# Kernel tuning notes

Hardware: AMD Instinct MI355X
Metric: run time of the kernel (lower is better)

Reference implementation:

```python
import jax, jax.numpy as jnp
import numpy as np


def setup_inputs() -> dict:
    key = jax.random.key(0)
    k1, k2, k3 = jax.random.split(key, 3)
    B, N, C_IN, C_OUT = 8, 2048, 128, 64
    x = jax.random.normal(k1, (B, N, C_IN), dtype=jnp.float32)
    # Linear(c_in, c_out): weight [c_out, c_in], bias [c_out]
    W_adj = jax.random.normal(k2, (C_OUT, C_IN), dtype=jnp.float32) * (1.0 / np.sqrt(C_IN))
    b_adj = jax.random.normal(k3, (C_OUT,), dtype=jnp.float32) * 0.01
    return {"x": x, "W_adj": W_adj, "b_adj": b_adj}


def reference(x, W_adj, b_adj):
    # e_x = adj_projection(x): [B, N, C_out]
    e_x = jnp.einsum("bnc,oc->bno", x, W_adj) + b_adj
    # The original loop/concat builds all (i, j) pairs and takes per-pair
    # inner products; this is exactly the Gram matrix e_x @ e_x^T.
    lp = jax.nn.relu(jnp.tanh(jnp.einsum("bic,bjc->bij", e_x, e_x)))  # [B, N, N]
    num_neighbours = x.shape[1]
    node_feats = jnp.einsum("bij,bjc->bic", lp, e_x) / num_neighbours
    return node_feats, lp
```

## Files before the change

### kernel.cpp

```cpp
#include <hip/hip_runtime.h>
#include <hip/hip_bf16.h>


#define B_    8
#define N_    2048
#define D_    64
#define CIN_  128

typedef __bf16 bf16x8 __attribute__((ext_vector_type(8)));
typedef float f32x4  __attribute__((ext_vector_type(4)));
typedef float f32x16 __attribute__((ext_vector_type(16)));

union FragU { uint4 u; bf16x8 f; };

static __device__ __forceinline__ bf16x8 ld_frag(const __hip_bfloat16* p) {
    FragU fu; fu.u = *reinterpret_cast<const uint4*>(p); return fu.f;
}

static __device__ __forceinline__ void split8(const float* p, bf16x8& hi, bf16x8& lo) {
    const float4 a = *reinterpret_cast<const float4*>(p);
    const float4 b = *reinterpret_cast<const float4*>(p + 4);
    const float v[8] = {a.x, a.y, a.z, a.w, b.x, b.y, b.z, b.w};
#pragma unroll
    for (int i = 0; i < 8; i++) {
        const __bf16 h = (__bf16)v[i];
        hi[i] = h;
        lo[i] = (__bf16)(v[i] - (float)h);
    }
}

__global__ __launch_bounds__(256) void ex_kernel(
    const float* __restrict__ x,
    const float* __restrict__ W,
    const float* __restrict__ bias,
    __hip_bfloat16* __restrict__ e_hi,
    __hip_bfloat16* __restrict__ e_lo,
    __hip_bfloat16* __restrict__ e_hiT)
{
    __shared__ __align__(16) __hip_bfloat16 sEh[64 * 72];
    __shared__ __align__(16) __hip_bfloat16 sEl[64 * 72];
    __shared__ __align__(16) __hip_bfloat16 sEt[64 * 72];

    const int tid  = threadIdx.x;
    const int w    = tid >> 6;
    const int lane = tid & 63;
    const int quad = lane >> 4;
    const int l16  = lane & 15;
    const int gr0  = blockIdx.x * 64;
    const int m0   = gr0 + w * 16;

    const float* xrow = x + (size_t)(m0 + l16) * CIN_;
    bf16x8 ah[4], al[4];
#pragma unroll
    for (int ks = 0; ks < 4; ks++)
        split8(xrow + ks * 32 + quad * 8, ah[ks], al[ks]);

    f32x4 acc[4];
#pragma unroll
    for (int nt = 0; nt < 4; nt++) acc[nt] = f32x4{0.f, 0.f, 0.f, 0.f};

#pragma unroll
    for (int ks = 0; ks < 4; ks++) {
#pragma unroll
        for (int nt = 0; nt < 4; nt++) {
            bf16x8 wh, wl;
            split8(W + (size_t)(nt * 16 + l16) * CIN_ + ks * 32 + quad * 8, wh, wl);
            acc[nt] = __builtin_amdgcn_mfma_f32_16x16x32_bf16(ah[ks], wh, acc[nt], 0, 0, 0);
            acc[nt] = __builtin_amdgcn_mfma_f32_16x16x32_bf16(ah[ks], wl, acc[nt], 0, 0, 0);
            acc[nt] = __builtin_amdgcn_mfma_f32_16x16x32_bf16(al[ks], wh, acc[nt], 0, 0, 0);
        }
    }

#pragma unroll
    for (int nt = 0; nt < 4; nt++) {
        const int chan = nt * 16 + l16;
        const float bv = bias[chan];
#pragma unroll
        for (int i = 0; i < 4; i++) {
            const int rl = w * 16 + quad * 4 + i;
            const float e = acc[nt][i] + bv;
            const __hip_bfloat16 hi = __float2bfloat16(e);
            const __hip_bfloat16 lo = __float2bfloat16(e - __bfloat162float(hi));
            sEh[rl * 72 + chan] = hi;
            sEl[rl * 72 + chan] = lo;
            sEt[chan * 72 + rl] = hi;
        }
    }
    __syncthreads();

    const int bt = gr0 >> 11, ir0 = gr0 & (N_ - 1);
#pragma unroll
    for (int p = 0; p < 2; p++) {
        const int q = tid + p * 256;
        const int r = q >> 3, c = (q & 7) * 8;
        *(uint4*)(e_hi + (size_t)(gr0 + r) * D_ + c)  = *(const uint4*)(sEh + r * 72 + c);
        *(uint4*)(e_lo + (size_t)(gr0 + r) * D_ + c)  = *(const uint4*)(sEl + r * 72 + c);
        *(uint4*)(e_hiT + ((size_t)bt * D_ + r) * N_ + ir0 + c) = *(const uint4*)(sEt + r * 72 + c);
    }
}

#define LT 136

__global__ __launch_bounds__(512) void fused_kernel(
    const __hip_bfloat16* __restrict__ e_hi,
    const __hip_bfloat16* __restrict__ e_lo,
    const __hip_bfloat16* __restrict__ e_hiT,
    float* __restrict__ out)
{
    __shared__ __align__(16) __hip_bfloat16 sLp[64 * LT];
    __shared__ __align__(16) float sO[8 * 32 * 64];

    const int b   = blockIdx.x;
    const int i0  = blockIdx.y * 64;
    const int tid = threadIdx.x;
    const int w = tid >> 6, lane = tid & 63;
    const int l32 = lane & 31, half = lane >> 5;
    const int quad = lane >> 4, l16 = lane & 15;
    const int g2 = w >> 2, h2 = w & 3;

    const __hip_bfloat16* eih = e_hi + (size_t)(b * N_ + i0 + g2 * 32 + l32) * D_;
    const __hip_bfloat16* eil = e_lo + (size_t)(b * N_ + i0 + g2 * 32 + l32) * D_;
    bf16x8 ahi[4], alo[4];
#pragma unroll
    for (int ks = 0; ks < 4; ks++) {
        ahi[ks] = ld_frag(eih + ks * 16 + half * 8);
        alo[ks] = ld_frag(eil + ks * 16 + half * 8);
    }

    f32x4 o[2][4];
#pragma unroll
    for (int mt = 0; mt < 2; mt++)
#pragma unroll
        for (int nt = 0; nt < 4; nt++) o[mt][nt] = f32x4{0.f, 0.f, 0.f, 0.f};

    float* lp_out = out + (size_t)B_ * N_ * D_;

    const __hip_bfloat16* ejh_base = e_hi + (size_t)(b * N_ + h2 * 32 + l32) * D_;
    const __hip_bfloat16* ejl_base = e_lo + (size_t)(b * N_ + h2 * 32 + l32) * D_;

    bf16x8 bh[4], bl[4];
#pragma unroll
    for (int ks = 0; ks < 4; ks++) {
        bh[ks] = ld_frag(ejh_base + ks * 16 + half * 8);
        bl[ks] = ld_frag(ejl_base + ks * 16 + half * 8);
    }

    for (int jt = 0; jt < 16; jt++) {
        const int j0 = jt * 128;

        f32x16 s = {};
#pragma unroll
        for (int ks = 0; ks < 4; ks++) {
            s = __builtin_amdgcn_mfma_f32_32x32x16_bf16(ahi[ks], bh[ks], s, 0, 0, 0);
            s = __builtin_amdgcn_mfma_f32_32x32x16_bf16(ahi[ks], bl[ks], s, 0, 0, 0);
            s = __builtin_amdgcn_mfma_f32_32x32x16_bf16(alo[ks], bh[ks], s, 0, 0, 0);
        }

        const int jn = ((jt + 1) & 15) * 128;
#pragma unroll
        for (int ks = 0; ks < 4; ks++) {
            bh[ks] = ld_frag(ejh_base + (size_t)jn * D_ + ks * 16 + half * 8);
            bl[ks] = ld_frag(ejl_base + (size_t)jn * D_ + ks * 16 + half * 8);
        }

        bf16x8 bfr[4];
#pragma unroll
        for (int nt = 0; nt < 4; nt++)
            bfr[nt] = ld_frag(e_hiT + ((size_t)b * D_ + nt * 16 + l16) * N_
                              + j0 + h2 * 32 + quad * 8);

#pragma unroll
        for (int r = 0; r < 16; r++) {
            const int rl = (r & 3) + 8 * (r >> 2) + 4 * half;
            const float tc = fmaxf(s[r], 0.0f);
            const float z = __builtin_amdgcn_exp2f(tc * -2.8853900817779268f);
            const float v = (1.0f - z) * __builtin_amdgcn_rcpf(1.0f + z);
            __builtin_nontemporal_store(
                v, lp_out + (size_t)(b * N_ + i0 + g2 * 32 + rl) * N_ + j0 + h2 * 32 + l32);
            sLp[(g2 * 32 + rl) * LT + h2 * 32 + l32] = __float2bfloat16(v);
        }

        __builtin_amdgcn_s_waitcnt(0xc07f);

#pragma unroll
        for (int mt = 0; mt < 2; mt++) {
            const bf16x8 a = ld_frag(sLp + (g2 * 32 + mt * 16 + l16) * LT + h2 * 32 + quad * 8);
#pragma unroll
            for (int nt = 0; nt < 4; nt++)
                o[mt][nt] = __builtin_amdgcn_mfma_f32_16x16x32_bf16(a, bfr[nt], o[mt][nt], 0, 0, 0);
        }
    }

    __syncthreads();
#pragma unroll
    for (int mt = 0; mt < 2; mt++)
#pragma unroll
        for (int nt = 0; nt < 4; nt++)
#pragma unroll
            for (int i = 0; i < 4; i++)
                sO[w * 2048 + (mt * 16 + quad * 4 + i) * 64 + nt * 16 + l16] = o[mt][nt][i];
    __syncthreads();
#pragma unroll
    for (int p = 0; p < 8; p++) {
        const int q = tid + p * 512;
        const int row = q >> 6, chan = q & 63;
        const int gg = row >> 5, rl = row & 31;
        float v = 0.f;
#pragma unroll
        for (int hh = 0; hh < 4; hh++)
            v += sO[(gg * 4 + hh) * 2048 + rl * 64 + chan];
        out[(size_t)(b * N_ + i0 + row) * D_ + chan] = v * (1.0f / 2048.0f);
    }
}

extern "C" void kernel_launch(void* const* d_in, const int* in_sizes, int n_in,
                              void* d_out, int out_size, void* d_ws, size_t ws_size,
                              hipStream_t stream) {
    const float* x    = (const float*)d_in[0];
    const float* W    = (const float*)d_in[1];
    const float* bias = (const float*)d_in[2];
    float* out = (float*)d_out;

    __hip_bfloat16* e_hi  = (__hip_bfloat16*)d_ws;
    __hip_bfloat16* e_lo  = e_hi + (size_t)B_ * N_ * D_;
    __hip_bfloat16* e_hiT = e_lo + (size_t)B_ * N_ * D_;

    ex_kernel<<<dim3(256), dim3(256), 0, stream>>>(x, W, bias, e_hi, e_lo, e_hiT);
    fused_kernel<<<dim3(8, 32), dim3(512), 0, stream>>>(e_hi, e_lo, e_hiT, out);
}
```

Before: 188.7 us.

## Stage lp tile in fp32 shared memory and write it with coalesced vector stores

The fused kernel now handles 32 rows per block and 512 columns per iteration, with each wave owning 64 columns. The lp values are kept in a double-buffered fp32 shared tile and written to global memory as coalesced 16-byte nontemporal row stores, replacing scattered scalar stores. The grid doubles to 512 blocks and the bf16 conversion moves into the A-fragment load. The cost is much more shared memory per block (about 132 KB), which likely limits occupancy to one block per CU, plus an added __syncthreads per iteration.

```diff
diff --git a/kernel.cpp b/kernel.cpp
--- a/kernel.cpp
+++ b/kernel.cpp
@@ -7,6 +7,12 @@
 #define D_    64
 #define CIN_  128
 
+#define BI    32
+#define BJ    512
+#define NJT   (N_ / BJ)
+#define LW    516
+#define SLPB  (BI * LW)
+
 typedef __bf16 bf16x8 __attribute__((ext_vector_type(8)));
 typedef float f32x4  __attribute__((ext_vector_type(4)));
 typedef float f32x16 __attribute__((ext_vector_type(16)));
@@ -27,6 +33,15 @@
         hi[i] = h;
         lo[i] = (__bf16)(v[i] - (float)h);
     }
+}
+
+static __device__ __forceinline__ bf16x8 cvt8(const float* p) {
+    const float4 a = *reinterpret_cast<const float4*>(p);
+    const float4 b = *reinterpret_cast<const float4*>(p + 4);
+    bf16x8 r;
+    r[0] = (__bf16)a.x; r[1] = (__bf16)a.y; r[2] = (__bf16)a.z; r[3] = (__bf16)a.w;
+    r[4] = (__bf16)b.x; r[5] = (__bf16)b.y; r[6] = (__bf16)b.z; r[7] = (__bf16)b.w;
+    return r;
 }
 
 __global__ __launch_bounds__(256) void ex_kernel(
@@ -99,27 +114,24 @@
     }
 }
 
-#define LT 136
-
 __global__ __launch_bounds__(512) void fused_kernel(
     const __hip_bfloat16* __restrict__ e_hi,
     const __hip_bfloat16* __restrict__ e_lo,
     const __hip_bfloat16* __restrict__ e_hiT,
     float* __restrict__ out)
 {
-    __shared__ __align__(16) __hip_bfloat16 sLp[64 * LT];
-    __shared__ __align__(16) float sO[8 * 32 * 64];
+    __shared__ __align__(16) float smem[2 * SLPB];
 
     const int b   = blockIdx.x;
-    const int i0  = blockIdx.y * 64;
+    const int i0  = blockIdx.y * BI;
     const int tid = threadIdx.x;
     const int w = tid >> 6, lane = tid & 63;
     const int l32 = lane & 31, half = lane >> 5;
     const int quad = lane >> 4, l16 = lane & 15;
-    const int g2 = w >> 2, h2 = w & 3;
-
-    const __hip_bfloat16* eih = e_hi + (size_t)(b * N_ + i0 + g2 * 32 + l32) * D_;
-    const __hip_bfloat16* eil = e_lo + (size_t)(b * N_ + i0 + g2 * 32 + l32) * D_;
+    const int cb = w * 64;
+
+    const __hip_bfloat16* eih = e_hi + (size_t)(b * N_ + i0 + l32) * D_;
+    const __hip_bfloat16* eil = e_lo + (size_t)(b * N_ + i0 + l32) * D_;
     bf16x8 ahi[4], alo[4];
 #pragma unroll
     for (int ks = 0; ks < 4; ks++) {
@@ -135,80 +147,107 @@
 
     float* lp_out = out + (size_t)B_ * N_ * D_;
 
-    const __hip_bfloat16* ejh_base = e_hi + (size_t)(b * N_ + h2 * 32 + l32) * D_;
-    const __hip_bfloat16* ejl_base = e_lo + (size_t)(b * N_ + h2 * 32 + l32) * D_;
-
-    bf16x8 bh[4], bl[4];
-#pragma unroll
-    for (int ks = 0; ks < 4; ks++) {
-        bh[ks] = ld_frag(ejh_base + ks * 16 + half * 8);
-        bl[ks] = ld_frag(ejl_base + ks * 16 + half * 8);
-    }
-
-    for (int jt = 0; jt < 16; jt++) {
-        const int j0 = jt * 128;
-
-        f32x16 s = {};
+    const __hip_bfloat16* ejh_base = e_hi + (size_t)(b * N_ + cb + l32) * D_;
+    const __hip_bfloat16* ejl_base = e_lo + (size_t)(b * N_ + cb + l32) * D_;
+
+    bf16x8 bh[2][4], bl[2][4];
+#pragma unroll
+    for (int st = 0; st < 2; st++)
 #pragma unroll
         for (int ks = 0; ks < 4; ks++) {
-            s = __builtin_amdgcn_mfma_f32_32x32x16_bf16(ahi[ks], bh[ks], s, 0, 0, 0);
-            s = __builtin_amdgcn_mfma_f32_32x32x16_bf16(ahi[ks], bl[ks], s, 0, 0, 0);
-            s = __builtin_amdgcn_mfma_f32_32x32x16_bf16(alo[ks], bh[ks], s, 0, 0, 0);
-        }
-
-        const int jn = ((jt + 1) & 15) * 128;
-#pragma unroll
-        for (int ks = 0; ks < 4; ks++) {
-            bh[ks] = ld_frag(ejh_base + (size_t)jn * D_ + ks * 16 + half * 8);
-            bl[ks] = ld_frag(ejl_base + (size_t)jn * D_ + ks * 16 + half * 8);
-        }
-
-        bf16x8 bfr[4];
+            bh[st][ks] = ld_frag(ejh_base + (size_t)st * 32 * D_ + ks * 16 + half * 8);
+            bl[st][ks] = ld_frag(ejl_base + (size_t)st * 32 * D_ + ks * 16 + half * 8);
+        }
+
+    int cur = 0;
+    for (int jt = 0; jt < NJT; jt++) {
+        const int j0 = jt * BJ;
+        float* sLp = smem + cur * SLPB;
+
+        f32x16 s[2] = {f32x16{}, f32x16{}};
+#pragma unroll
+        for (int st = 0; st < 2; st++)
+#pragma unroll
+            for (int ks = 0; ks < 4; ks++) {
+                s[st] = __builtin_amdgcn_mfma_f32_32x32x16_bf16(ahi[ks], bh[st][ks], s[st], 0, 0, 0);
+                s[st] = __builtin_amdgcn_mfma_f32_32x32x16_bf16(ahi[ks], bl[st][ks], s[st], 0, 0, 0);
+                s[st] = __builtin_amdgcn_mfma_f32_32x32x16_bf16(alo[ks], bh[st][ks], s[st], 0, 0, 0);
+            }
+
+        const int jn = ((jt + 1) & (NJT - 1)) * BJ;
+#pragma unroll
+        for (int st = 0; st < 2; st++)
+#pragma unroll
+            for (int ks = 0; ks < 4; ks++) {
+                bh[st][ks] = ld_frag(ejh_base + (size_t)(jn + st * 32) * D_ + ks * 16 + half * 8);
+                bl[st][ks] = ld_frag(ejl_base + (size_t)(jn + st * 32) * D_ + ks * 16 + half * 8);
+            }
+
+        bf16x8 bfr[2][4];
+#pragma unroll
+        for (int ks = 0; ks < 2; ks++)
+#pragma unroll
+            for (int nt = 0; nt < 4; nt++)
+                bfr[ks][nt] = ld_frag(e_hiT + ((size_t)b * D_ + nt * 16 + l16) * N_
+                                      + j0 + cb + ks * 32 + quad * 8);
+
+#pragma unroll
+        for (int st = 0; st < 2; st++)
+#pragma unroll
+            for (int r = 0; r < 16; r++) {
+                const int rl = (r & 3) + 8 * (r >> 2) + 4 * half;
+                const float tc = fmaxf(s[st][r], 0.0f);
+                const float z = __builtin_amdgcn_exp2f(tc * -2.8853900817779268f);
+                sLp[rl * LW + cb + st * 32 + l32] =
+                    (1.0f - z) * __builtin_amdgcn_rcpf(1.0f + z);
+            }
+
+        __builtin_amdgcn_s_waitcnt(0xc07f);
+
+#pragma unroll
+        for (int ks = 0; ks < 2; ks++)
+#pragma unroll
+            for (int mt = 0; mt < 2; mt++) {
+                const bf16x8 a = cvt8(sLp + (mt * 16 + l16) * LW + cb + ks * 32 + quad * 8);
+#pragma unroll
+                for (int nt = 0; nt < 4; nt++)
+                    o[mt][nt] = __builtin_amdgcn_mfma_f32_16x16x32_bf16(a, bfr[ks][nt], o[mt][nt], 0, 0, 0);
+            }
+
+        __syncthreads();
+
+        {
+            const int r = tid >> 4, c0 = (tid & 15);
+            float* dst = lp_out + (size_t)(b * N_ + i0 + r) * N_ + j0;
+            const float* src = sLp + r * LW;
+#pragma unroll
+            for (int p = 0; p < 8; p++) {
+                const int c = (c0 + p * 16) * 4;
+                const f32x4 vv = *(const f32x4*)(src + c);
+                __builtin_nontemporal_store(vv, (f32x4*)(dst + c));
+            }
+        }
+        cur ^= 1;
+    }
+
+    __syncthreads();
+    float* sO = smem;
+#pragma unroll
+    for (int mt = 0; mt < 2; mt++)
 #pragma unroll
         for (int nt = 0; nt < 4; nt++)
-            bfr[nt] = ld_frag(e_hiT + ((size_t)b * D_ + nt * 16 + l16) * N_
-                              + j0 + h2 * 32 + quad * 8);
-
-#pragma unroll
-        for (int r = 0; r < 16; r++) {
-            const int rl = (r & 3) + 8 * (r >> 2) + 4 * half;
-            const float tc = fmaxf(s[r], 0.0f);
-            const float z = __builtin_amdgcn_exp2f(tc * -2.8853900817779268f);
-            const float v = (1.0f - z) * __builtin_amdgcn_rcpf(1.0f + z);
-            __builtin_nontemporal_store(
-                v, lp_out + (size_t)(b * N_ + i0 + g2 * 32 + rl) * N_ + j0 + h2 * 32 + l32);
-            sLp[(g2 * 32 + rl) * LT + h2 * 32 + l32] = __float2bfloat16(v);
-        }
-
-        __builtin_amdgcn_s_waitcnt(0xc07f);
-
-#pragma unroll
-        for (int mt = 0; mt < 2; mt++) {
-            const bf16x8 a = ld_frag(sLp + (g2 * 32 + mt * 16 + l16) * LT + h2 * 32 + quad * 8);
-#pragma unroll
-            for (int nt = 0; nt < 4; nt++)
-                o[mt][nt] = __builtin_amdgcn_mfma_f32_16x16x32_bf16(a, bfr[nt], o[mt][nt], 0, 0, 0);
-        }
-    }
-
+#pragma unroll
+            for (int i = 0; i < 4; i++)
+                sO[w * (BI * 64) + (mt * 16 + quad * 4 + i) * 64 + nt * 16 + l16] = o[mt][nt][i];
     __syncthreads();
 #pragma unroll
-    for (int mt = 0; mt < 2; mt++)
-#pragma unroll
-        for (int nt = 0; nt < 4; nt++)
-#pragma unroll
-            for (int i = 0; i < 4; i++)
-                sO[w * 2048 + (mt * 16 + quad * 4 + i) * 64 + nt * 16 + l16] = o[mt][nt][i];
-    __syncthreads();
-#pragma unroll
-    for (int p = 0; p < 8; p++) {
+    for (int p = 0; p < 4; p++) {
         const int q = tid + p * 512;
         const int row = q >> 6, chan = q & 63;
-        const int gg = row >> 5, rl = row & 31;
         float v = 0.f;
 #pragma unroll
-        for (int hh = 0; hh < 4; hh++)
-            v += sO[(gg * 4 + hh) * 2048 + rl * 64 + chan];
+        for (int hh = 0; hh < 8; hh++)
+            v += sO[hh * (BI * 64) + row * 64 + chan];
         out[(size_t)(b * N_ + i0 + row) * D_ + chan] = v * (1.0f / 2048.0f);
     }
 }
@@ -226,5 +265,5 @@
     __hip_bfloat16* e_hiT = e_lo + (size_t)B_ * N_ * D_;
 
     ex_kernel<<<dim3(256), dim3(256), 0, stream>>>(x, W, bias, e_hi, e_lo, e_hiT);
-    fused_kernel<<<dim3(8, 32), dim3(512), 0, stream>>>(e_hi, e_lo, e_hiT, out);
-}
+    fused_kernel<<<dim3(8, 64), dim3(512), 0, stream>>>(e_hi, e_lo, e_hiT, out);
+}
```

Result: slower. 203.4 us (+7.8%).
